# Kernel tuning notes

Measured on AMD Instinct MI355X. Metric: run time of the kernel, lower is better.

## Reference

```python
import jax, jax.numpy as jnp
import numpy as np

D_K = 128
NEG_BIG = 1e32  # matches torch's -1e+32 additive mask (finite in fp32)


def setup_inputs() -> dict:
    key = jax.random.key(0)
    kq, kk, kv, kqp, kkp = jax.random.split(key, 5)
    B, M, N, d_k, d_v = 8, 2048, 2048, D_K, 128
    return {
        "queries": jax.random.normal(kq, (B, M, d_k), dtype=jnp.float32),
        "keys": jax.random.normal(kk, (B, N, d_k), dtype=jnp.float32),
        "values": jax.random.normal(kv, (B, N, d_v), dtype=jnp.float32),
        "q_pres": jax.random.randint(kqp, (B, M), 0, 2, dtype=jnp.int32),
        "k_pres": jax.random.randint(kkp, (B, N), 0, 2, dtype=jnp.int32),
    }


def reference(queries, keys, values, q_pres, k_pres):
    # routing: [B, M, N] = Q K^T with multiplicative presence masking
    routing = jnp.einsum("bmd,bnd->bmn", queries, keys)
    qp = q_pres.astype(jnp.float32)  # [B, M]
    kp = k_pres.astype(jnp.float32)  # [B, N]
    routing = routing * qp[:, :, None]
    routing = routing * kp[:, None, :]
    # additive -1e32 mask for absent keys, then scaled softmax over N
    routing = routing - (1.0 - kp[:, None, :]) * NEG_BIG
    routing = jax.nn.softmax(routing / np.sqrt(D_K).astype(np.float32), axis=-1)
    return jnp.einsum("bmn,bnv->bmv", routing, values)
```

## Files before the change

### kernel.cpp

```cpp
#include <hip/hip_runtime.h>
#include <cstddef>
#include <cstdint>

#define SEQ_M 2048
#define SEQ_N 2048
#define DKV 128
#define BN 64
#define NCH 4
#define CHKEYS (SEQ_N / NCH)
#define NKT 32
#define MT2 16
#define NREC (NCH * 8 * MT2)

typedef _Float16 f16x8 __attribute__((ext_vector_type(8)));
typedef _Float16 f16x4 __attribute__((ext_vector_type(4)));
typedef float f32x4 __attribute__((ext_vector_type(4)));

#if defined(__has_builtin)
#if __has_builtin(__builtin_amdgcn_exp2f)
#define EXP2F(x) __builtin_amdgcn_exp2f(x)
#else
#define EXP2F(x) exp2f(x)
#endif
#else
#define EXP2F(x) exp2f(x)
#endif

#define SM_SCALE 0.12751745f
#define BIG_NEG 1.2751745e31f
#define MSHIFT 8.0f

#define KH_OFF 0
#define VH_OFF (256 * 8192)
#define P16_OFF (2 * 256 * 8192)
#define L_BYTE_OFF ((size_t)(P16_OFF + (size_t)NREC * 16384) * 2)
#define WS_NEED (L_BYTE_OFF + (size_t)NREC * 128 * 4)

#define AS1 __attribute__((address_space(1)))
#define AS3 __attribute__((address_space(3)))

__device__ __forceinline__ void copy16(const void* g, void* lds_base,
                                       void* lds_lane) {
#if defined(__has_builtin) && __has_builtin(__builtin_amdgcn_global_load_lds)
  __builtin_amdgcn_global_load_lds((const AS1 void*)g, (AS3 void*)lds_base, 16,
                                   0, 0);
  (void)lds_lane;
#else
  *(f16x8*)lds_lane = *(const f16x8*)g;
#endif
}

__global__ __launch_bounds__(256) void prep(const float* __restrict__ Kg,
                                            const float* __restrict__ Vg,
                                            _Float16* __restrict__ Kh,
                                            _Float16* __restrict__ Vh) {
  const int T = blockIdx.x >> 2;
  const int kind = blockIdx.x & 1;
  const int half = (blockIdx.x >> 1) & 1;
  const int b = T >> 5, nt = T & 31;
  const int t = threadIdx.x;
  if (kind == 0) {
    const float* Kb = Kg + ((size_t)b * SEQ_N + nt * 64) * DKV;
    _Float16* Kt_ = Kh + (size_t)T * 8192;
#pragma unroll
    for (int i = 0; i < 2; ++i) {
      const int idx = half * 512 + i * 256 + t;
      const int c = idx & 15, key = idx >> 4;
      const float* src = Kb + key * DKV + c * 8;
      const float4 a0 = *(const float4*)src;
      const float4 a1 = *(const float4*)(src + 4);
      f16x8 h;
      h[0] = (_Float16)a0.x; h[1] = (_Float16)a0.y;
      h[2] = (_Float16)a0.z; h[3] = (_Float16)a0.w;
      h[4] = (_Float16)a1.x; h[5] = (_Float16)a1.y;
      h[6] = (_Float16)a1.z; h[7] = (_Float16)a1.w;
      *(f16x8*)&Kt_[c * 512 + key * 8] = h;
    }
  } else {
    const float* Vb = Vg + ((size_t)b * SEQ_N + nt * 64) * DKV;
    _Float16* Vt_ = Vh + (size_t)T * 8192;
#pragma unroll
    for (int i = 0; i < 2; ++i) {
      const int idx = half * 512 + i * 256 + t;
      const int vcol = idx & 127, g = idx >> 7;
      f16x8 h;
#pragma unroll
      for (int j = 0; j < 8; ++j)
        h[j] = (_Float16)Vb[(size_t)(g * 8 + j) * DKV + vcol];
      *(f16x8*)&Vt_[vcol * 64 + ((g ^ (vcol & 7)) * 8)] = h;
    }
  }
}

__global__ __launch_bounds__(256, 2) void attn_core5(
    const _Float16* __restrict__ Kh, const _Float16* __restrict__ Vh,
    const float* __restrict__ Qg, const int* __restrict__ QPg,
    const int* __restrict__ KPg, _Float16* __restrict__ P16,
    float* __restrict__ Lw) {
  __shared__ _Float16 smem[16384 + 4 * 2304];
  _Float16* const Kt = smem;
  _Float16* const Vt = smem + 8192;

  const int tid = threadIdx.x;
  const int w = tid >> 6;
  const int lane = tid & 63;
  const int q16 = lane & 15;
  const int quad = lane >> 4;
  _Float16* const Pl = smem + 16384 + w * 2304;

  const int b = blockIdx.x & 7;
  const int rest = blockIdx.x >> 3;
  const int mt = rest & 15;
  const int chk = rest >> 4;

  const int qrowA = mt * 128 + w * 32 + q16;
  const float* qptrA = Qg + ((size_t)b * SEQ_M + qrowA) * DKV;
  const float* qptrB = qptrA + 16 * DKV;
  const float qsA = QPg[b * SEQ_M + qrowA] ? 1.0f : 0.0f;
  const float qsB = QPg[b * SEQ_M + qrowA + 16] ? 1.0f : 0.0f;
  f16x8 qfA[4], qfB[4];
#pragma unroll
  for (int kc = 0; kc < 4; ++kc) {
    const float4 a0 = *(const float4*)(qptrA + kc * 32 + quad * 8);
    const float4 a1 = *(const float4*)(qptrA + kc * 32 + quad * 8 + 4);
    f16x8 h;
    h[0] = (_Float16)(a0.x * qsA); h[1] = (_Float16)(a0.y * qsA);
    h[2] = (_Float16)(a0.z * qsA); h[3] = (_Float16)(a0.w * qsA);
    h[4] = (_Float16)(a1.x * qsA); h[5] = (_Float16)(a1.y * qsA);
    h[6] = (_Float16)(a1.z * qsA); h[7] = (_Float16)(a1.w * qsA);
    qfA[kc] = h;
    const float4 b0 = *(const float4*)(qptrB + kc * 32 + quad * 8);
    const float4 b1 = *(const float4*)(qptrB + kc * 32 + quad * 8 + 4);
    f16x8 g;
    g[0] = (_Float16)(b0.x * qsB); g[1] = (_Float16)(b0.y * qsB);
    g[2] = (_Float16)(b0.z * qsB); g[3] = (_Float16)(b0.w * qsB);
    g[4] = (_Float16)(b1.x * qsB); g[5] = (_Float16)(b1.y * qsB);
    g[6] = (_Float16)(b1.z * qsB); g[7] = (_Float16)(b1.w * qsB);
    qfB[kc] = g;
  }

  f32x4 oA[8], oB[8];
#pragma unroll
  for (int vt = 0; vt < 8; ++vt) {
    oA[vt] = (f32x4){0.f, 0.f, 0.f, 0.f};
    oB[vt] = (f32x4){0.f, 0.f, 0.f, 0.f};
  }
  float plA = 0.f, plB = 0.f;

  for (int ti = 0; ti < CHKEYS / BN; ++ti) {
    const int nt = chk * 8 + ti;
    __syncthreads();

    {
      const char* gsrc =
          (w < 2) ? (const char*)(Kh + (size_t)(b * NKT + nt) * 8192) + w * 8192
                  : (const char*)(Vh + (size_t)(b * NKT + nt) * 8192) +
                        (w - 2) * 8192;
      char* ldst = (w < 2) ? (char*)Kt + w * 8192 : (char*)Vt + (w - 2) * 8192;
#pragma unroll
      for (int r = 0; r < 8; ++r)
        copy16(gsrc + r * 1024 + lane * 16, ldst + r * 1024,
               ldst + r * 1024 + lane * 16);
    }
    const unsigned long long kmask =
        __ballot(KPg[(size_t)b * SEQ_N + nt * 64 + lane] != 0);
    __syncthreads();

    f32x4 stA[4], stB[4];
#pragma unroll
    for (int t = 0; t < 4; ++t) {
      stA[t] = (f32x4){0.f, 0.f, 0.f, 0.f};
      stB[t] = (f32x4){0.f, 0.f, 0.f, 0.f};
    }
#pragma unroll
    for (int kc = 0; kc < 4; ++kc) {
      const f16x8 qvA = qfA[kc];
      const f16x8 qvB = qfB[kc];
#pragma unroll
      for (int t = 0; t < 4; ++t) {
        const f16x8 kf =
            *(const f16x8*)&Kt[((kc * 4 + quad) * 64 + t * 16 + q16) * 8];
        stA[t] = __builtin_amdgcn_mfma_f32_16x16x32_f16(kf, qvA, stA[t], 0, 0, 0);
        stB[t] = __builtin_amdgcn_mfma_f32_16x16x32_f16(kf, qvB, stB[t], 0, 0, 0);
      }
    }

    float pA[16], pB[16];
#pragma unroll
    for (int t = 0; t < 4; ++t)
#pragma unroll
      for (int r = 0; r < 4; ++r) {
        const int key = t * 16 + quad * 4 + r;
        const bool on = (kmask >> key) & 1ull;
        const float eA = EXP2F(stA[t][r] * SM_SCALE - MSHIFT);
        const float eB = EXP2F(stB[t][r] * SM_SCALE - MSHIFT);
        const float vA = on ? eA : 0.f;
        const float vB = on ? eB : 0.f;
        pA[t * 4 + r] = vA; plA += vA;
        pB[t * 4 + r] = vB; plB += vB;
      }

#pragma unroll
    for (int t = 0; t < 4; ++t) {
      f16x4 pwA, pwB;
#pragma unroll
      for (int r = 0; r < 4; ++r) {
        pwA[r] = (_Float16)pA[t * 4 + r];
        pwB[r] = (_Float16)pB[t * 4 + r];
      }
      *(f16x4*)&Pl[q16 * 72 + t * 16 + quad * 4] = pwA;
      *(f16x4*)&Pl[(16 + q16) * 72 + t * 16 + quad * 4] = pwB;
    }
    const f16x8 pfA0 = *(const f16x8*)&Pl[q16 * 72 + quad * 8];
    const f16x8 pfA1 = *(const f16x8*)&Pl[q16 * 72 + 32 + quad * 8];
    const f16x8 pfB0 = *(const f16x8*)&Pl[(16 + q16) * 72 + quad * 8];
    const f16x8 pfB1 = *(const f16x8*)&Pl[(16 + q16) * 72 + 32 + quad * 8];

#pragma unroll
    for (int vt = 0; vt < 8; ++vt) {
      const int vcol = vt * 16 + q16;
      const f16x8 v0 =
          *(const f16x8*)&Vt[vcol * 64 + ((quad ^ (vcol & 7)) * 8)];
      const f16x8 v1 =
          *(const f16x8*)&Vt[vcol * 64 + (((quad + 4) ^ (vcol & 7)) * 8)];
      oA[vt] = __builtin_amdgcn_mfma_f32_16x16x32_f16(pfA0, v0, oA[vt], 0, 0, 0);
      oA[vt] = __builtin_amdgcn_mfma_f32_16x16x32_f16(pfA1, v1, oA[vt], 0, 0, 0);
      oB[vt] = __builtin_amdgcn_mfma_f32_16x16x32_f16(pfB0, v0, oB[vt], 0, 0, 0);
      oB[vt] = __builtin_amdgcn_mfma_f32_16x16x32_f16(pfB1, v1, oB[vt], 0, 0, 0);
    }
  }

  plA += __shfl_xor(plA, 16); plA += __shfl_xor(plA, 32);
  plB += __shfl_xor(plB, 16); plB += __shfl_xor(plB, 32);
  float liA[4], liB[4];
#pragma unroll
  for (int r = 0; r < 4; ++r) {
    liA[r] = 1.0f / __shfl(plA, quad * 4 + r);
    liB[r] = 1.0f / __shfl(plB, quad * 4 + r);
  }
  const int rec = (chk * 8 + b) * MT2 + mt;
  _Float16* obA = P16 + (size_t)rec * 16384 + (size_t)(w * 32) * 128;
  _Float16* obB = obA + 16 * 128;
#pragma unroll
  for (int vt = 0; vt < 8; ++vt)
#pragma unroll
    for (int r = 0; r < 4; ++r) {
      obA[(quad * 4 + r) * 128 + vt * 16 + q16] =
          (_Float16)(oA[vt][r] * liA[r]);
      obB[(quad * 4 + r) * 128 + vt * 16 + q16] =
          (_Float16)(oB[vt][r] * liB[r]);
    }
  if (quad == 0) {
    float* lr = Lw + (size_t)rec * 128;
    lr[w * 32 + q16] = plA;
    lr[w * 32 + 16 + q16] = plB;
  }
}

__global__ __launch_bounds__(256) void attn_combine3(
    const _Float16* __restrict__ P16, const float* __restrict__ Lw,
    float* __restrict__ Og) {
  const int t = threadIdx.x;
  const int b = blockIdx.x & 7;
  const int mt = blockIdx.x >> 3;
  __shared__ float lsh[NCH][128];
#pragma unroll
  for (int i = 0; i < 2; ++i) {
    const int idx = i * 256 + t;
    const int c = idx >> 7, row = idx & 127;
    lsh[c][row] = Lw[(size_t)((c * 8 + b) * MT2 + mt) * 128 + row];
  }
  __syncthreads();
  const int colh = (t & 31) * 4;
  const int rg = t >> 5;
  const _Float16* recO[NCH];
#pragma unroll
  for (int c = 0; c < NCH; ++c)
    recO[c] = P16 + (size_t)((c * 8 + b) * MT2 + mt) * 16384;
  float* outb = Og + ((size_t)b * SEQ_M + mt * 128) * DKV;
#pragma unroll
  for (int rr = 0; rr < 16; ++rr) {
    const int row = rr * 8 + rg;
    float lt = 0.f;
#pragma unroll
    for (int c = 0; c < NCH; ++c) lt += lsh[c][row];
    const float inv = 1.0f / lt;
    f32x4 acc = (f32x4){0.f, 0.f, 0.f, 0.f};
#pragma unroll
    for (int c = 0; c < NCH; ++c) {
      const float wc = lsh[c][row];
      const f16x4 v = *(const f16x4*)(recO[c] + (size_t)row * 128 + colh);
      acc[0] += wc * (float)v[0]; acc[1] += wc * (float)v[1];
      acc[2] += wc * (float)v[2]; acc[3] += wc * (float)v[3];
    }
    f32x4 r;
    r[0] = acc[0] * inv; r[1] = acc[1] * inv;
    r[2] = acc[2] * inv; r[3] = acc[3] * inv;
    *(f32x4*)(outb + (size_t)row * DKV + colh) = r;
  }
}

__global__ __launch_bounds__(256) void attn_fallback(
    const float* __restrict__ Qg, const float* __restrict__ Kg,
    const float* __restrict__ Vg, const int* __restrict__ QPg,
    const int* __restrict__ KPg, float* __restrict__ Og) {
  __shared__ _Float16 smem[16 * 65 * 8 + 128 * 72];
  _Float16* const Kt = smem;
  _Float16* const Vt = smem + 16 * 65 * 8;
  const int tid = threadIdx.x;
  const int w = tid >> 6;
  const int lane = tid & 63;
  const int q16 = lane & 15;
  const int quad = lane >> 4;
  _Float16* const Pl = smem + w * (16 * 72);
  const int b = blockIdx.x & 7;
  const int mb = (blockIdx.x >> 3) * 64;
  const int qrow = mb + w * 16 + q16;
  const float* qptr = Qg + ((size_t)b * SEQ_M + qrow) * DKV;
  const float qs = QPg[b * SEQ_M + qrow] ? 1.0f : 0.0f;
  f16x8 qf[4];
#pragma unroll
  for (int kc = 0; kc < 4; ++kc) {
    const float4 a0 = *(const float4*)(qptr + kc * 32 + quad * 8);
    const float4 a1 = *(const float4*)(qptr + kc * 32 + quad * 8 + 4);
    f16x8 h;
    h[0] = (_Float16)(a0.x * qs); h[1] = (_Float16)(a0.y * qs);
    h[2] = (_Float16)(a0.z * qs); h[3] = (_Float16)(a0.w * qs);
    h[4] = (_Float16)(a1.x * qs); h[5] = (_Float16)(a1.y * qs);
    h[6] = (_Float16)(a1.z * qs); h[7] = (_Float16)(a1.w * qs);
    qf[kc] = h;
  }
  f32x4 o[8];
#pragma unroll
  for (int vt = 0; vt < 8; ++vt) o[vt] = (f32x4){0.f, 0.f, 0.f, 0.f};
  float m_run = -3.0e38f, l_run = 0.f;
  const int kn = tid >> 2, ks = (tid & 3) * 32;
  const int vg = tid >> 3, vk = (tid & 7) * 8;
  for (int n0 = 0; n0 < SEQ_N; n0 += BN) {
    __syncthreads();
    {
      const float* kp_ = Kg + ((size_t)b * SEQ_N + n0 + kn) * DKV + ks;
#pragma unroll
      for (int c2 = 0; c2 < 4; ++c2) {
        const float4 a0 = *(const float4*)(kp_ + c2 * 8);
        const float4 a1 = *(const float4*)(kp_ + c2 * 8 + 4);
        f16x8 h;
        h[0] = (_Float16)a0.x; h[1] = (_Float16)a0.y;
        h[2] = (_Float16)a0.z; h[3] = (_Float16)a0.w;
        h[4] = (_Float16)a1.x; h[5] = (_Float16)a1.y;
        h[6] = (_Float16)a1.z; h[7] = (_Float16)a1.w;
        *(f16x8*)&Kt[(((ks >> 3) + c2) * 65 + kn) * 8] = h;
      }
    }
    {
      const float* vp0 = Vg + ((size_t)b * SEQ_N + n0 + vk) * DKV + vg * 4;
      float4 vv[8];
#pragma unroll
      for (int j = 0; j < 8; ++j) vv[j] = *(const float4*)(vp0 + (size_t)j * DKV);
#pragma unroll
      for (int i = 0; i < 4; ++i) {
        f16x8 h;
#pragma unroll
        for (int j = 0; j < 8; ++j) h[j] = (_Float16)(((const float*)&vv[j])[i]);
        *(f16x8*)&Vt[(vg * 4 + i) * 72 + vk] = h;
      }
    }
    const unsigned long long kmask =
        __ballot(KPg[(size_t)b * SEQ_N + n0 + lane] != 0);
    __syncthreads();
    f32x4 st[4];
#pragma unroll
    for (int t = 0; t < 4; ++t) st[t] = (f32x4){0.f, 0.f, 0.f, 0.f};
#pragma unroll
    for (int kc = 0; kc < 4; ++kc) {
      const f16x8 qv = qf[kc];
#pragma unroll
      for (int t = 0; t < 4; ++t) {
        const f16x8 kf =
            *(const f16x8*)&Kt[((kc * 4 + quad) * 65 + t * 16 + q16) * 8];
        st[t] = __builtin_amdgcn_mfma_f32_16x16x32_f16(kf, qv, st[t], 0, 0, 0);
      }
    }
    float s2[16];
    float mx = -3.0e38f;
#pragma unroll
    for (int t = 0; t < 4; ++t)
#pragma unroll
      for (int r = 0; r < 4; ++r) {
        const int key = t * 16 + quad * 4 + r;
        const float v =
            ((kmask >> key) & 1ull) ? st[t][r] * SM_SCALE : -BIG_NEG;
        s2[t * 4 + r] = v;
        mx = fmaxf(mx, v);
      }
    mx = fmaxf(mx, __shfl_xor(mx, 16));
    mx = fmaxf(mx, __shfl_xor(mx, 32));
    const float mnew = fmaxf(m_run, mx);
    const float alpha = EXP2F(m_run - mnew);
    m_run = mnew;
    float p[16];
    float psum = 0.f;
#pragma unroll
    for (int i = 0; i < 16; ++i) {
      p[i] = EXP2F(s2[i] - mnew);
      psum += p[i];
    }
    psum += __shfl_xor(psum, 16);
    psum += __shfl_xor(psum, 32);
    l_run = l_run * alpha + psum;
    float arow[4];
#pragma unroll
    for (int r = 0; r < 4; ++r) arow[r] = __shfl(alpha, quad * 4 + r);
#pragma unroll
    for (int vt = 0; vt < 8; ++vt) {
      o[vt][0] *= arow[0]; o[vt][1] *= arow[1];
      o[vt][2] *= arow[2]; o[vt][3] *= arow[3];
    }
    __syncthreads();
#pragma unroll
    for (int t = 0; t < 4; ++t) {
      f16x4 pw;
      pw[0] = (_Float16)p[t * 4 + 0];
      pw[1] = (_Float16)p[t * 4 + 1];
      pw[2] = (_Float16)p[t * 4 + 2];
      pw[3] = (_Float16)p[t * 4 + 3];
      *(f16x4*)&Pl[q16 * 72 + t * 16 + quad * 4] = pw;
    }
    const f16x8 pf0 = *(const f16x8*)&Pl[q16 * 72 + quad * 8];
    const f16x8 pf1 = *(const f16x8*)&Pl[q16 * 72 + 32 + quad * 8];
#pragma unroll
    for (int vt = 0; vt < 8; ++vt) {
      const f16x8 v0 = *(const f16x8*)&Vt[(vt * 16 + q16) * 72 + quad * 8];
      o[vt] = __builtin_amdgcn_mfma_f32_16x16x32_f16(pf0, v0, o[vt], 0, 0, 0);
      const f16x8 v1 = *(const f16x8*)&Vt[(vt * 16 + q16) * 72 + 32 + quad * 8];
      o[vt] = __builtin_amdgcn_mfma_f32_16x16x32_f16(pf1, v1, o[vt], 0, 0, 0);
    }
  }
  float linv[4];
#pragma unroll
  for (int r = 0; r < 4; ++r) linv[r] = 1.0f / __shfl(l_run, quad * 4 + r);
  float* obase = Og + ((size_t)b * SEQ_M + mb + w * 16) * DKV;
#pragma unroll
  for (int vt = 0; vt < 8; ++vt)
#pragma unroll
    for (int r = 0; r < 4; ++r)
      obase[(size_t)(quad * 4 + r) * DKV + vt * 16 + q16] = o[vt][r] * linv[r];
}

extern "C" void kernel_launch(void* const* d_in, const int* in_sizes, int n_in,
                              void* d_out, int out_size, void* d_ws,
                              size_t ws_size, hipStream_t stream) {
  const float* Q = (const float*)d_in[0];
  const float* K = (const float*)d_in[1];
  const float* V = (const float*)d_in[2];
  const int* QP = (const int*)d_in[3];
  const int* KP = (const int*)d_in[4];
  float* O = (float*)d_out;
  if (ws_size >= WS_NEED) {
    _Float16* wsh = (_Float16*)d_ws;
    _Float16* Kh = wsh + KH_OFF;
    _Float16* Vh = wsh + VH_OFF;
    _Float16* P16 = wsh + P16_OFF;
    float* Lw = (float*)((char*)d_ws + L_BYTE_OFF);
    prep<<<dim3(1024), dim3(256), 0, stream>>>(K, V, Kh, Vh);
    attn_core5<<<dim3(8 * MT2 * NCH), dim3(256), 0, stream>>>(
        Kh, Vh, Q, QP, KP, P16, Lw);
    attn_combine3<<<dim3(8 * MT2), dim3(256), 0, stream>>>(P16, Lw, O);
  } else {
    attn_fallback<<<dim3(8 * 32), dim3(256), 0, stream>>>(Q, K, V, QP, KP, O);
  }
}
```

Measured before the change: 110.9 us.

## Double-buffer K/V tiles and fuse split-K combine via last-block atomic election

The core kernel now double-buffers K/V tiles in LDS, issuing the next tile's async copy before computing the current one. This removes one barrier per iteration and hides global-load latency. The presence masks for all eight tiles are ballotted up front, and the P staging buffer is halved by reusing it for the A and B rows in turn. The separate combine kernel is removed: each block bumps an atomic counter and the last chunk block for a row tile does the cross-chunk reduction, which saves a launch at the cost of a memset and more LDS per block (the occupancy hint is dropped).

```diff
diff --git a/kernel.cpp b/kernel.cpp
--- a/kernel.cpp
+++ b/kernel.cpp
@@ -34,7 +34,8 @@
 #define VH_OFF (256 * 8192)
 #define P16_OFF (2 * 256 * 8192)
 #define L_BYTE_OFF ((size_t)(P16_OFF + (size_t)NREC * 16384) * 2)
-#define WS_NEED (L_BYTE_OFF + (size_t)NREC * 128 * 4)
+#define FLAGS_BYTE_OFF (L_BYTE_OFF + (size_t)NREC * 128 * 4)
+#define WS_NEED (FLAGS_BYTE_OFF + 128 * sizeof(int))
 
 #define AS1 __attribute__((address_space(1)))
 #define AS3 __attribute__((address_space(3)))
@@ -92,21 +93,21 @@
   }
 }
 
-__global__ __launch_bounds__(256, 2) void attn_core5(
+__global__ __launch_bounds__(256) void attn_core6(
     const _Float16* __restrict__ Kh, const _Float16* __restrict__ Vh,
     const float* __restrict__ Qg, const int* __restrict__ QPg,
     const int* __restrict__ KPg, _Float16* __restrict__ P16,
-    float* __restrict__ Lw) {
-  __shared__ _Float16 smem[16384 + 4 * 2304];
-  _Float16* const Kt = smem;
-  _Float16* const Vt = smem + 8192;
+    float* __restrict__ Lw, int* __restrict__ Flags,
+    float* __restrict__ Og) {
+  __shared__ _Float16 smem[4 * 8192 + 4 * 1152];
+  __shared__ int elect;
 
   const int tid = threadIdx.x;
   const int w = tid >> 6;
   const int lane = tid & 63;
   const int q16 = lane & 15;
   const int quad = lane >> 4;
-  _Float16* const Pl = smem + 16384 + w * 2304;
+  _Float16* const Pl = smem + 32768 + w * 1152;
 
   const int b = blockIdx.x & 7;
   const int rest = blockIdx.x >> 3;
@@ -139,6 +140,11 @@
     qfB[kc] = g;
   }
 
+  unsigned long long km[8];
+#pragma unroll
+  for (int t = 0; t < 8; ++t)
+    km[t] = __ballot(KPg[(size_t)b * SEQ_N + (chk * 8 + t) * 64 + lane] != 0);
+
   f32x4 oA[8], oB[8];
 #pragma unroll
   for (int vt = 0; vt < 8; ++vt) {
@@ -147,24 +153,29 @@
   }
   float plA = 0.f, plB = 0.f;
 
-  for (int ti = 0; ti < CHKEYS / BN; ++ti) {
-    const int nt = chk * 8 + ti;
+#define STAGE(buf, nt)                                                        \
+  {                                                                           \
+    const char* gsrc =                                                        \
+        (w < 2)                                                               \
+            ? (const char*)(Kh + (size_t)(b * NKT + (nt)) * 8192) + w * 8192  \
+            : (const char*)(Vh + (size_t)(b * NKT + (nt)) * 8192) +           \
+                  (w - 2) * 8192;                                             \
+    char* ldst = (w < 2) ? (char*)(smem + (buf)*8192) + w * 8192              \
+                         : (char*)(smem + 16384 + (buf)*8192) + (w - 2) * 8192; \
+    _Pragma("unroll") for (int r = 0; r < 8; ++r)                             \
+        copy16(gsrc + r * 1024 + lane * 16, ldst + r * 1024,                  \
+               ldst + r * 1024 + lane * 16);                                  \
+  }
+
+  STAGE(0, chk * 8);
+
+  for (int ti = 0; ti < 8; ++ti) {
+    const int cur = ti & 1;
     __syncthreads();
-
-    {
-      const char* gsrc =
-          (w < 2) ? (const char*)(Kh + (size_t)(b * NKT + nt) * 8192) + w * 8192
-                  : (const char*)(Vh + (size_t)(b * NKT + nt) * 8192) +
-                        (w - 2) * 8192;
-      char* ldst = (w < 2) ? (char*)Kt + w * 8192 : (char*)Vt + (w - 2) * 8192;
-#pragma unroll
-      for (int r = 0; r < 8; ++r)
-        copy16(gsrc + r * 1024 + lane * 16, ldst + r * 1024,
-               ldst + r * 1024 + lane * 16);
-    }
-    const unsigned long long kmask =
-        __ballot(KPg[(size_t)b * SEQ_N + nt * 64 + lane] != 0);
-    __syncthreads();
+    if (ti < 7) STAGE(cur ^ 1, chk * 8 + ti + 1);
+
+    const _Float16* const Kt = smem + cur * 8192;
+    const _Float16* const Vt = smem + 16384 + cur * 8192;
 
     f32x4 stA[4], stB[4];
 #pragma unroll
@@ -185,6 +196,7 @@
       }
     }
 
+    const unsigned long long kmask = km[ti];
     float pA[16], pB[16];
 #pragma unroll
     for (int t = 0; t < 4; ++t)
@@ -202,19 +214,22 @@
 
 #pragma unroll
     for (int t = 0; t < 4; ++t) {
-      f16x4 pwA, pwB;
-#pragma unroll
-      for (int r = 0; r < 4; ++r) {
-        pwA[r] = (_Float16)pA[t * 4 + r];
-        pwB[r] = (_Float16)pB[t * 4 + r];
-      }
-      *(f16x4*)&Pl[q16 * 72 + t * 16 + quad * 4] = pwA;
-      *(f16x4*)&Pl[(16 + q16) * 72 + t * 16 + quad * 4] = pwB;
+      f16x4 pw;
+#pragma unroll
+      for (int r = 0; r < 4; ++r) pw[r] = (_Float16)pA[t * 4 + r];
+      *(f16x4*)&Pl[q16 * 72 + t * 16 + quad * 4] = pw;
     }
     const f16x8 pfA0 = *(const f16x8*)&Pl[q16 * 72 + quad * 8];
     const f16x8 pfA1 = *(const f16x8*)&Pl[q16 * 72 + 32 + quad * 8];
-    const f16x8 pfB0 = *(const f16x8*)&Pl[(16 + q16) * 72 + quad * 8];
-    const f16x8 pfB1 = *(const f16x8*)&Pl[(16 + q16) * 72 + 32 + quad * 8];
+#pragma unroll
+    for (int t = 0; t < 4; ++t) {
+      f16x4 pw;
+#pragma unroll
+      for (int r = 0; r < 4; ++r) pw[r] = (_Float16)pB[t * 4 + r];
+      *(f16x4*)&Pl[q16 * 72 + t * 16 + quad * 4] = pw;
+    }
+    const f16x8 pfB0 = *(const f16x8*)&Pl[q16 * 72 + quad * 8];
+    const f16x8 pfB1 = *(const f16x8*)&Pl[q16 * 72 + 32 + quad * 8];
 
 #pragma unroll
     for (int vt = 0; vt < 8; ++vt) {
@@ -255,48 +270,47 @@
     lr[w * 32 + q16] = plA;
     lr[w * 32 + 16 + q16] = plB;
   }
-}
-
-__global__ __launch_bounds__(256) void attn_combine3(
-    const _Float16* __restrict__ P16, const float* __restrict__ Lw,
-    float* __restrict__ Og) {
-  const int t = threadIdx.x;
-  const int b = blockIdx.x & 7;
-  const int mt = blockIdx.x >> 3;
-  __shared__ float lsh[NCH][128];
-#pragma unroll
-  for (int i = 0; i < 2; ++i) {
-    const int idx = i * 256 + t;
-    const int c = idx >> 7, row = idx & 127;
-    lsh[c][row] = Lw[(size_t)((c * 8 + b) * MT2 + mt) * 128 + row];
-  }
+
+  __threadfence();
+  if (tid == 0) elect = atomicAdd(&Flags[b * MT2 + mt], 1);
   __syncthreads();
-  const int colh = (t & 31) * 4;
-  const int rg = t >> 5;
-  const _Float16* recO[NCH];
-#pragma unroll
-  for (int c = 0; c < NCH; ++c)
-    recO[c] = P16 + (size_t)((c * 8 + b) * MT2 + mt) * 16384;
-  float* outb = Og + ((size_t)b * SEQ_M + mt * 128) * DKV;
-#pragma unroll
-  for (int rr = 0; rr < 16; ++rr) {
-    const int row = rr * 8 + rg;
-    float lt = 0.f;
-#pragma unroll
-    for (int c = 0; c < NCH; ++c) lt += lsh[c][row];
-    const float inv = 1.0f / lt;
-    f32x4 acc = (f32x4){0.f, 0.f, 0.f, 0.f};
-#pragma unroll
-    for (int c = 0; c < NCH; ++c) {
-      const float wc = lsh[c][row];
-      const f16x4 v = *(const f16x4*)(recO[c] + (size_t)row * 128 + colh);
-      acc[0] += wc * (float)v[0]; acc[1] += wc * (float)v[1];
-      acc[2] += wc * (float)v[2]; acc[3] += wc * (float)v[3];
-    }
-    f32x4 r;
-    r[0] = acc[0] * inv; r[1] = acc[1] * inv;
-    r[2] = acc[2] * inv; r[3] = acc[3] * inv;
-    *(f32x4*)(outb + (size_t)row * DKV + colh) = r;
+  if (elect == NCH - 1) {
+    __threadfence();
+    float* lsh = (float*)smem;
+#pragma unroll
+    for (int i = 0; i < 2; ++i) {
+      const int idx = i * 256 + tid;
+      const int c = idx >> 7, row = idx & 127;
+      lsh[idx] = Lw[(size_t)((c * 8 + b) * MT2 + mt) * 128 + row];
+    }
+    __syncthreads();
+    const int colh = (tid & 31) * 4;
+    const int rg = tid >> 5;
+    const _Float16* recO[NCH];
+#pragma unroll
+    for (int c = 0; c < NCH; ++c)
+      recO[c] = P16 + (size_t)((c * 8 + b) * MT2 + mt) * 16384;
+    float* outb = Og + ((size_t)b * SEQ_M + mt * 128) * DKV;
+#pragma unroll
+    for (int rr = 0; rr < 16; ++rr) {
+      const int row = rr * 8 + rg;
+      float lt = 0.f;
+#pragma unroll
+      for (int c = 0; c < NCH; ++c) lt += lsh[c * 128 + row];
+      const float inv = 1.0f / lt;
+      f32x4 acc = (f32x4){0.f, 0.f, 0.f, 0.f};
+#pragma unroll
+      for (int c = 0; c < NCH; ++c) {
+        const float wc = lsh[c * 128 + row];
+        const f16x4 v = *(const f16x4*)(recO[c] + (size_t)row * 128 + colh);
+        acc[0] += wc * (float)v[0]; acc[1] += wc * (float)v[1];
+        acc[2] += wc * (float)v[2]; acc[3] += wc * (float)v[3];
+      }
+      f32x4 r;
+      r[0] = acc[0] * inv; r[1] = acc[1] * inv;
+      r[2] = acc[2] * inv; r[3] = acc[3] * inv;
+      *(f32x4*)(outb + (size_t)row * DKV + colh) = r;
+    }
   }
 }
 
@@ -462,10 +476,11 @@
     _Float16* Vh = wsh + VH_OFF;
     _Float16* P16 = wsh + P16_OFF;
     float* Lw = (float*)((char*)d_ws + L_BYTE_OFF);
+    int* Flags = (int*)((char*)d_ws + FLAGS_BYTE_OFF);
+    hipMemsetAsync(Flags, 0, 128 * sizeof(int), stream);
     prep<<<dim3(1024), dim3(256), 0, stream>>>(K, V, Kh, Vh);
-    attn_core5<<<dim3(8 * MT2 * NCH), dim3(256), 0, stream>>>(
-        Kh, Vh, Q, QP, KP, P16, Lw);
-    attn_combine3<<<dim3(8 * MT2), dim3(256), 0, stream>>>(P16, Lw, O);
+    attn_core6<<<dim3(8 * MT2 * NCH), dim3(256), 0, stream>>>(
+        Kh, Vh, Q, QP, KP, P16, Lw, Flags, O);
   } else {
     attn_fallback<<<dim3(8 * 32), dim3(256), 0, stream>>>(Q, K, V, QP, KP, O);
   }
```

Measured after the change: 187.5 us. 1.69x slower.
